# Performance work log

Measured on AMD Instinct MI355X. Metric: run time of the kernel, lower is better.

The kernel has to match this reference:

```python
import jax, jax.numpy as jnp
import numpy as np

RATE = 0.001  # matches init kwarg `rate`


def _hebbian_layer(vi, w, b, c1w, c1b, c2w, c2b, batch_num):
    # vi: (B, I), w: (O, I), b: (O,)
    vj = jax.nn.relu(vi @ w.T + b)  # (B, O) == relu(old_vj)
    # meta-MLP over the broadcasted (B, O, I) grid with 3 input channels
    # (input_stack, weight_stack, output_stack); conv1 is 1x1 so it is a
    # per-element linear map 3 -> H. We fuse the broadcast into the matmul
    # instead of materializing the stacked (B, 3, O, I) tensor.
    # c1w: (H, 3), c1b: (H,)
    h = jax.nn.relu(
        vi[:, None, :, None] * c1w[:, 0]
        + w[None, :, :, None] * c1w[:, 1]
        + vj[:, :, None, None] * c1w[:, 2]
        + c1b
    )  # (B, O, I, H)
    # conv2: H -> 1, then squeeze; scale by rate / batch_num
    shift = (h @ c2w + c2b) * (RATE / batch_num)  # (B, O, I)
    # out = old_vj + sum(input_stack * shift, dim=2)
    out = vj + jnp.sum(vi[:, None, :] * shift, axis=2)  # (B, O)
    # NOTE: torch also does layer.data += mean(shift, dim=0) as a stateful
    # side effect; it does not affect this forward pass's return value.
    return out


def setup_inputs() -> dict:
    key = jax.random.key(0)
    ks = jax.random.split(key, 9)
    B, I, Hd, O, MH = 8, 1024, 2048, 512, 8
    inp = {
        "x": jax.random.normal(ks[0], (B, I), dtype=jnp.float32),
        "w1": jax.random.normal(ks[1], (Hd, I), dtype=jnp.float32) * 0.02,
        "b1": jax.random.normal(ks[2], (Hd,), dtype=jnp.float32) * 0.02,
        "w2": jax.random.normal(ks[3], (O, Hd), dtype=jnp.float32) * 0.02,
        "b2": jax.random.normal(ks[4], (O,), dtype=jnp.float32) * 0.02,
        "c1w": jax.random.normal(ks[5], (MH, 3), dtype=jnp.float32) * 0.5,
        "c1b": jax.random.normal(ks[6], (MH,), dtype=jnp.float32) * 0.5,
        "c2w": jax.random.normal(ks[7], (MH,), dtype=jnp.float32) * 0.5,
        "c2b": jax.random.normal(ks[8], (), dtype=jnp.float32) * 0.5,
        "batch_num": 1,
    }
    return inp


def reference(x, w1, b1, w2, b2, c1w, c1b, c2w, c2b, batch_num):
    out = _hebbian_layer(x, w1, b1, c1w, c1b, c2w, c2b, batch_num)
    out = _hebbian_layer(out, w2, b2, c1w, c1b, c2w, c2b, batch_num)
    return out
```

## Files before the change

### kernel.cpp

```cpp
#include <hip/hip_runtime.h>

#define RATE 0.001f

typedef float f2 __attribute__((ext_vector_type(2)));
typedef float f4 __attribute__((ext_vector_type(4)));

static __device__ __forceinline__ f2 splat2(float v) { f2 r; r.x = v; r.y = v; return r; }

template<int I>
__global__ __launch_bounds__(256) void hebb_layer(
    const float* __restrict__ vi,
    const float* __restrict__ w,
    const float* __restrict__ bias,
    const float* __restrict__ c1w,
    const float* __restrict__ c1b,
    const float* __restrict__ c2w,
    const float* __restrict__ c2b_p,
    const int*   __restrict__ bn_p,
    float* __restrict__ out,
    int O)
{
    const int o    = blockIdx.x;
    const int tid  = threadIdx.x;
    const int lane = tid & 63;
    const int wid  = tid >> 6;
    const int b0   = wid * 2;

    f2 p2[4], q2[4], r2[4], cb2[4], c22[4];
#pragma unroll
    for (int j = 0; j < 4; ++j) {
        p2[j].x  = c1w[(2*j)*3 + 0];  p2[j].y  = c1w[(2*j+1)*3 + 0];
        q2[j].x  = c1w[(2*j)*3 + 1];  q2[j].y  = c1w[(2*j+1)*3 + 1];
        r2[j].x  = c1w[(2*j)*3 + 2];  r2[j].y  = c1w[(2*j+1)*3 + 2];
        cb2[j].x = c1b[2*j];          cb2[j].y = c1b[2*j+1];
        c22[j].x = c2w[2*j];          c22[j].y = c2w[2*j+1];
    }
    const float c2b   = *c2b_p;
    const float scale = RATE / (float)(*bn_p);
    const float bo    = bias[o];

    const float* __restrict__ wrow  = w  + (size_t)o  * I;
    const float* __restrict__ arow0 = vi + (size_t)b0 * I;
    const float* __restrict__ arow1 = arow0 + I;

    constexpr int ITERS = I / 256;

    float dot0 = 0.f, dot1 = 0.f, ss0 = 0.f, ss1 = 0.f;
    for (int it = 0; it < ITERS; ++it) {
        const int base = it * 256 + lane * 4;
        const f4 wv = *(const f4*)(wrow  + base);
        const f4 a0 = *(const f4*)(arow0 + base);
        const f4 a1 = *(const f4*)(arow1 + base);
#pragma unroll
        for (int e = 0; e < 4; ++e) {
            dot0 = fmaf(a0[e], wv[e], dot0);
            dot1 = fmaf(a1[e], wv[e], dot1);
            ss0 += a0[e];
            ss1 += a1[e];
        }
    }
#pragma unroll
    for (int off = 1; off < 64; off <<= 1) {
        dot0 += __shfl_xor(dot0, off, 64);
        dot1 += __shfl_xor(dot1, off, 64);
        ss0  += __shfl_xor(ss0,  off, 64);
        ss1  += __shfl_xor(ss1,  off, 64);
    }
    const float vj0 = fmaxf(dot0 + bo, 0.f);
    const float vj1 = fmaxf(dot1 + bo, 0.f);

    f2 k20[4], k21[4];
#pragma unroll
    for (int j = 0; j < 4; ++j) {
        k20[j] = splat2(vj0) * r2[j] + cb2[j];
        k21[j] = splat2(vj1) * r2[j] + cb2[j];
    }

    f2 acc0 = splat2(0.f), acc1 = splat2(0.f);
    for (int it = 0; it < ITERS; ++it) {
        const int base = it * 256 + lane * 4;
        const f4 wv4 = *(const f4*)(wrow  + base);
        const f4 a04 = *(const f4*)(arow0 + base);
        const f4 a14 = *(const f4*)(arow1 + base);
#pragma unroll
        for (int e = 0; e < 4; ++e) {
            const f2 wvE = splat2(wv4[e]);
            const f2 a0E = splat2(a04[e]);
            const f2 a1E = splat2(a14[e]);
            f2 t0 = splat2(0.f), t1 = splat2(0.f);
#pragma unroll
            for (int j = 0; j < 4; ++j) {
                f2 z0 = wvE * q2[j] + k20[j];
                z0 = a0E * p2[j] + z0;
                const f2 u0 = __builtin_elementwise_max(z0, splat2(0.f));
                t0 = u0 * c22[j] + t0;
                f2 z1 = wvE * q2[j] + k21[j];
                z1 = a1E * p2[j] + z1;
                const f2 u1 = __builtin_elementwise_max(z1, splat2(0.f));
                t1 = u1 * c22[j] + t1;
            }
            acc0 = a0E * t0 + acc0;
            acc1 = a1E * t1 + acc1;
        }
    }
    float r0 = acc0.x + acc0.y;
    float r1 = acc1.x + acc1.y;
#pragma unroll
    for (int off = 1; off < 64; off <<= 1) {
        r0 += __shfl_xor(r0, off, 64);
        r1 += __shfl_xor(r1, off, 64);
    }

    if (lane == 0) {
        out[(size_t)(b0    ) * O + o] = vj0 + scale * (r0 + c2b * ss0);
        out[(size_t)(b0 + 1) * O + o] = vj1 + scale * (r1 + c2b * ss1);
    }
}

extern "C" void kernel_launch(void* const* d_in, const int* in_sizes, int n_in,
                              void* d_out, int out_size, void* d_ws, size_t ws_size,
                              hipStream_t stream) {
    const float* x   = (const float*)d_in[0];
    const float* w1  = (const float*)d_in[1];
    const float* b1  = (const float*)d_in[2];
    const float* w2  = (const float*)d_in[3];
    const float* b2  = (const float*)d_in[4];
    const float* c1w = (const float*)d_in[5];
    const float* c1b = (const float*)d_in[6];
    const float* c2w = (const float*)d_in[7];
    const float* c2b = (const float*)d_in[8];
    const int*   bn  = (const int*)d_in[9];

    float* out = (float*)d_out;
    float* mid = (float*)d_ws;

    hebb_layer<1024><<<2048, 256, 0, stream>>>(x,   w1, b1, c1w, c1b, c2w, c2b, bn, mid, 2048);
    hebb_layer<2048><<<512,  256, 0, stream>>>(mid, w2, b2, c1w, c1b, c2w, c2b, bn, out, 512);
}
```

Before: 102.9 us.

## Split vj matvec into separate kernel and stage activations in shared memory

New measurement: 113.0 us. +9.9%, slower.

```diff
diff --git a/kernel.cpp b/kernel.cpp
--- a/kernel.cpp
+++ b/kernel.cpp
@@ -8,10 +8,68 @@
 static __device__ __forceinline__ f2 splat2(float v) { f2 r; r.x = v; r.y = v; return r; }
 
 template<int I>
-__global__ __launch_bounds__(256) void hebb_layer(
+__global__ __launch_bounds__(256) void hebb_vj(
     const float* __restrict__ vi,
     const float* __restrict__ w,
     const float* __restrict__ bias,
+    float* __restrict__ vj_out,
+    float* __restrict__ S_out,
+    int O, int nOb)
+{
+    const int tid  = threadIdx.x;
+    const int lane = tid & 63;
+    const int wid  = tid >> 6;
+    constexpr int ITERS = I / 256;
+
+    if ((int)blockIdx.x >= nOb) {
+        const int row = ((int)blockIdx.x - nOb) * 4 + wid;
+        const float* __restrict__ a = vi + (size_t)row * I;
+        float s = 0.f;
+        for (int it = 0; it < ITERS; ++it) {
+            const f4 v = *(const f4*)(a + it * 256 + lane * 4);
+            s += (v.x + v.y) + (v.z + v.w);
+        }
+#pragma unroll
+        for (int off = 1; off < 64; off <<= 1) s += __shfl_xor(s, off, 64);
+        if (lane == 0) S_out[row] = s;
+        return;
+    }
+
+    const int o = (int)blockIdx.x * 4 + wid;
+    const float* __restrict__ wrow = w + (size_t)o * I;
+    const float bo = bias[o];
+
+    float dot[8];
+#pragma unroll
+    for (int b = 0; b < 8; ++b) dot[b] = 0.f;
+
+    for (int it = 0; it < ITERS; ++it) {
+        const int base = it * 256 + lane * 4;
+        const f4 wv = *(const f4*)(wrow + base);
+#pragma unroll
+        for (int b = 0; b < 8; ++b) {
+            const f4 a = *(const f4*)(vi + (size_t)b * I + base);
+#pragma unroll
+            for (int e = 0; e < 4; ++e) dot[b] = fmaf(a[e], wv[e], dot[b]);
+        }
+    }
+#pragma unroll
+    for (int b = 0; b < 8; ++b) {
+#pragma unroll
+        for (int off = 1; off < 64; off <<= 1) dot[b] += __shfl_xor(dot[b], off, 64);
+    }
+    if (lane == 0) {
+#pragma unroll
+        for (int b = 0; b < 8; ++b) vj_out[(size_t)b * O + o] = fmaxf(dot[b] + bo, 0.f);
+    }
+}
+
+template<int I>
+__global__ __launch_bounds__(256, 4) void hebb_main(
+    const float* __restrict__ vi,
+    const float* __restrict__ w,
+    const float* __restrict__ vjA,
+    const float* __restrict__ S,
     const float* __restrict__ c1w,
     const float* __restrict__ c1b,
     const float* __restrict__ c2w,
@@ -20,6 +78,8 @@
     float* __restrict__ out,
     int O)
 {
+    __shared__ float sA[8 * 1024];
+
     const int o    = blockIdx.x;
     const int tid  = threadIdx.x;
     const int lane = tid & 63;
@@ -37,37 +97,10 @@
     }
     const float c2b   = *c2b_p;
     const float scale = RATE / (float)(*bn_p);
-    const float bo    = bias[o];
-
-    const float* __restrict__ wrow  = w  + (size_t)o  * I;
-    const float* __restrict__ arow0 = vi + (size_t)b0 * I;
-    const float* __restrict__ arow1 = arow0 + I;
-
-    constexpr int ITERS = I / 256;
-
-    float dot0 = 0.f, dot1 = 0.f, ss0 = 0.f, ss1 = 0.f;
-    for (int it = 0; it < ITERS; ++it) {
-        const int base = it * 256 + lane * 4;
-        const f4 wv = *(const f4*)(wrow  + base);
-        const f4 a0 = *(const f4*)(arow0 + base);
-        const f4 a1 = *(const f4*)(arow1 + base);
-#pragma unroll
-        for (int e = 0; e < 4; ++e) {
-            dot0 = fmaf(a0[e], wv[e], dot0);
-            dot1 = fmaf(a1[e], wv[e], dot1);
-            ss0 += a0[e];
-            ss1 += a1[e];
-        }
-    }
-#pragma unroll
-    for (int off = 1; off < 64; off <<= 1) {
-        dot0 += __shfl_xor(dot0, off, 64);
-        dot1 += __shfl_xor(dot1, off, 64);
-        ss0  += __shfl_xor(ss0,  off, 64);
-        ss1  += __shfl_xor(ss1,  off, 64);
-    }
-    const float vj0 = fmaxf(dot0 + bo, 0.f);
-    const float vj1 = fmaxf(dot1 + bo, 0.f);
+    const float S0    = S[b0];
+    const float S1    = S[b0 + 1];
+    const float vj0   = vjA[(size_t)(b0    ) * O + o];
+    const float vj1   = vjA[(size_t)(b0 + 1) * O + o];
 
     f2 k20[4], k21[4];
 #pragma unroll
@@ -76,33 +109,48 @@
         k21[j] = splat2(vj1) * r2[j] + cb2[j];
     }
 
+    const float* __restrict__ wrow = w + (size_t)o * I;
+    constexpr int NC = I / 1024;
+
     f2 acc0 = splat2(0.f), acc1 = splat2(0.f);
-    for (int it = 0; it < ITERS; ++it) {
-        const int base = it * 256 + lane * 4;
-        const f4 wv4 = *(const f4*)(wrow  + base);
-        const f4 a04 = *(const f4*)(arow0 + base);
-        const f4 a14 = *(const f4*)(arow1 + base);
+
+    for (int c = 0; c < NC; ++c) {
+        if (c) __syncthreads();
 #pragma unroll
-        for (int e = 0; e < 4; ++e) {
-            const f2 wvE = splat2(wv4[e]);
-            const f2 a0E = splat2(a04[e]);
-            const f2 a1E = splat2(a14[e]);
-            f2 t0 = splat2(0.f), t1 = splat2(0.f);
+        for (int s = 0; s < 8; ++s) {
+            *(f4*)&sA[s * 1024 + tid * 4] =
+                *(const f4*)(vi + (size_t)s * I + c * 1024 + tid * 4);
+        }
+        __syncthreads();
+
+        for (int it = 0; it < 4; ++it) {
+            const int base = it * 256 + lane * 4;
+            const f4 wv4 = *(const f4*)(wrow + c * 1024 + base);
+            const f4 a04 = *(const f4*)&sA[b0 * 1024 + base];
+            const f4 a14 = *(const f4*)&sA[(b0 + 1) * 1024 + base];
 #pragma unroll
-            for (int j = 0; j < 4; ++j) {
-                f2 z0 = wvE * q2[j] + k20[j];
-                z0 = a0E * p2[j] + z0;
-                const f2 u0 = __builtin_elementwise_max(z0, splat2(0.f));
-                t0 = u0 * c22[j] + t0;
-                f2 z1 = wvE * q2[j] + k21[j];
-                z1 = a1E * p2[j] + z1;
-                const f2 u1 = __builtin_elementwise_max(z1, splat2(0.f));
-                t1 = u1 * c22[j] + t1;
+            for (int e = 0; e < 4; ++e) {
+                const f2 wvE = splat2(wv4[e]);
+                const f2 a0E = splat2(a04[e]);
+                const f2 a1E = splat2(a14[e]);
+                f2 t0 = splat2(0.f), t1 = splat2(0.f);
+#pragma unroll
+                for (int j = 0; j < 4; ++j) {
+                    f2 z0 = wvE * q2[j] + k20[j];
+                    z0 = a0E * p2[j] + z0;
+                    const f2 u0 = __builtin_elementwise_max(z0, splat2(0.f));
+                    t0 = u0 * c22[j] + t0;
+                    f2 z1 = wvE * q2[j] + k21[j];
+                    z1 = a1E * p2[j] + z1;
+                    const f2 u1 = __builtin_elementwise_max(z1, splat2(0.f));
+                    t1 = u1 * c22[j] + t1;
+                }
+                acc0 = a0E * t0 + acc0;
+                acc1 = a1E * t1 + acc1;
             }
-            acc0 = a0E * t0 + acc0;
-            acc1 = a1E * t1 + acc1;
         }
     }
+
     float r0 = acc0.x + acc0.y;
     float r1 = acc1.x + acc1.y;
 #pragma unroll
@@ -110,10 +158,9 @@
         r0 += __shfl_xor(r0, off, 64);
         r1 += __shfl_xor(r1, off, 64);
     }
-
     if (lane == 0) {
-        out[(size_t)(b0    ) * O + o] = vj0 + scale * (r0 + c2b * ss0);
-        out[(size_t)(b0 + 1) * O + o] = vj1 + scale * (r1 + c2b * ss1);
+        out[(size_t)(b0    ) * O + o] = vj0 + scale * (r0 + c2b * S0);
+        out[(size_t)(b0 + 1) * O + o] = vj1 + scale * (r1 + c2b * S1);
     }
 }
 
@@ -132,8 +179,16 @@
     const int*   bn  = (const int*)d_in[9];
 
     float* out = (float*)d_out;
-    float* mid = (float*)d_ws;
+    float* ws  = (float*)d_ws;
 
-    hebb_layer<1024><<<2048, 256, 0, stream>>>(x,   w1, b1, c1w, c1b, c2w, c2b, bn, mid, 2048);
-    hebb_layer<2048><<<512,  256, 0, stream>>>(mid, w2, b2, c1w, c1b, c2w, c2b, bn, out, 512);
+    float* vj1  = ws;
+    float* S1   = ws + 16384;
+    float* out1 = ws + 16400;
+    float* vj2  = ws + 32784;
+    float* S2   = ws + 36880;
+
+    hebb_vj<1024>  <<<2048/4 + 2, 256, 0, stream>>>(x, w1, b1, vj1, S1, 2048, 2048/4);
+    hebb_main<1024><<<2048,       256, 0, stream>>>(x, w1, vj1, S1, c1w, c1b, c2w, c2b, bn, out1, 2048);
+    hebb_vj<2048>  <<<512/4 + 2,  256, 0, stream>>>(out1, w2, b2, vj2, S2, 512, 512/4);
+    hebb_main<2048><<<512,        256, 0, stream>>>(out1, w2, vj2, S2, c1w, c1b, c2w, c2b, bn, out, 512);
 }
```
